# Kernel tuning notes

Hardware: AMD Instinct MI355X
Metric: run time of the kernel (lower is better)

## Reference

```python
import jax, jax.numpy as jnp
import numpy as np

N = 50000      # total nodes across batched graphs
E = 400000     # directed edges (before self-loops)
B = 256        # number of graphs / protein embeddings
F_IN = 78      # atom features (num_features_xd)
H1, F1 = 10, 78   # gcn1: heads=10, out=78 -> concat 780
F2 = 128       # gcn2 output_dim (heads=1)
EMB = 320      # PLM embed_dim
PLM = 128      # plm_layers[0]
BN_EPS = 1e-5


def setup_inputs() -> dict:
    key = jax.random.key(0)
    ks = jax.random.split(key, 30)
    g = lambda k, s, sc=0.05: (jax.random.normal(k, s, jnp.float32) * sc)
    inp = {
        'x': jax.random.normal(ks[0], (N, F_IN), jnp.float32),
        'edge_index': jax.random.randint(ks[1], (2, E), 0, N),
        # deterministic sorted assignment guarantees every graph id in [0,B) is populated
        'batch': (jnp.arange(N) * B) // N,
        'target_embedding': jax.random.normal(ks[2], (B, EMB), jnp.float32),
        # GATConv 1 (78 -> 78, heads=10, concat)
        'W1': g(ks[3], (F_IN, H1 * F1)), 'a1s': g(ks[4], (H1, F1)), 'a1d': g(ks[5], (H1, F1)), 'b1': g(ks[6], (H1 * F1,)),
        # GATConv 2 (780 -> 128, heads=1)
        'W2': g(ks[7], (H1 * F1, F2)), 'a2s': g(ks[8], (1, F2)), 'a2d': g(ks[9], (1, F2)), 'b2': g(ks[10], (F2,)),
        # fc_g1
        'Wg': g(ks[11], (F2, F2)), 'bg': g(ks[12], (F2,)),
        # PLM branch: Linear(320,128) + BatchNorm1d(128) in eval mode
        'Wxt': g(ks[13], (EMB, PLM)), 'bxt': g(ks[14], (PLM,)),
        'gamma': jnp.ones((PLM,), jnp.float32), 'beta': jnp.zeros((PLM,), jnp.float32),
        'rmean': g(ks[15], (PLM,)), 'rvar': jax.random.uniform(ks[16], (PLM,), jnp.float32, 0.5, 1.5),
        # head MLP
        'Wf1': g(ks[17], (F2 + PLM, 1024)), 'bf1': g(ks[18], (1024,)),
        'Wf2': g(ks[19], (1024, 256)), 'bf2': g(ks[20], (256,)),
        'Wo': g(ks[21], (256, 1)), 'bo': g(ks[22], (1,)),
    }
    return inp


def gat_conv(x, src, dst, W, a_s, a_d, b, n):
    """PyG-style GATConv (self-loops already included in src/dst)."""
    H, F = a_s.shape
    h = (x @ W).reshape(-1, H, F)                        # [n, H, F]
    e = jax.nn.leaky_relu((h * a_s).sum(-1)[src] + (h * a_d).sum(-1)[dst], 0.2)  # [e, H]
    m = jax.ops.segment_max(e, dst, num_segments=n)      # segment softmax over incoming edges
    p = jnp.exp(e - m[dst])
    denom = jax.ops.segment_sum(p, dst, num_segments=n)
    alpha = p / denom[dst]                               # [e, H]
    out = jax.ops.segment_sum(alpha[:, :, None] * h[src], dst, num_segments=n)  # [n, H, F]
    return out.reshape(-1, H * F) + b


def reference(x, edge_index, batch, target_embedding, W1, a1s, a1d, b1, W2, a2s, a2d, b2,
              Wg, bg, Wxt, bxt, gamma, beta, rmean, rvar, Wf1, bf1, Wf2, bf2, Wo, bo):
    n = x.shape[0]
    loop = jnp.arange(n)
    src = jnp.concatenate([edge_index[0], loop])   # add self-loops (GATConv default)
    dst = jnp.concatenate([edge_index[1], loop])
    h = jax.nn.elu(gat_conv(x, src, dst, W1, a1s, a1d, b1, n))      # [N, 780]
    h = jax.nn.relu(gat_conv(h, src, dst, W2, a2s, a2d, b2, n))     # [N, 128]
    g = jax.ops.segment_max(h, batch, num_segments=B)               # global max pool [B, 128]
    g = jax.nn.relu(g @ Wg + bg)
    xt = target_embedding @ Wxt + bxt
    xt = jax.nn.relu((xt - rmean) / jnp.sqrt(rvar + BN_EPS) * gamma + beta)  # BN eval
    xc = jnp.concatenate([g, xt], axis=1)                           # [B, 256]
    xc = jax.nn.relu(xc @ Wf1 + bf1)
    xc = jax.nn.relu(xc @ Wf2 + bf2)
    return xc @ Wo + bo                                             # [B, 1]
```

## Files before the change

kernel.cpp:

```cpp
#include <hip/hip_runtime.h>
#include <hip/hip_fp16.h>
#include <math.h>

static constexpr int F2 = 128, EMB = 320;

typedef _Float16 h8v __attribute__((ext_vector_type(8)));
typedef float f4v __attribute__((ext_vector_type(4)));

union F4H2 { float4 f; __half2 h[4]; };
union F2H2 { float2 f; __half2 h[2]; };

__device__ __forceinline__ __half2 shfl_xor_h2(__half2 v, int off) {
    union { __half2 h; float f; } u;
    u.h = v;
    u.f = __shfl_xor(u.f, off);
    return u.h;
}

__device__ __forceinline__ void esd(const int* src, const int* dst, int E, int e, int& s, int& d) {
    if (e < E) { s = src[e]; d = dst[e]; }
    else       { s = e - E; d = s; }
}

__global__ void k_count(const int* __restrict__ src, const int* __restrict__ dst, int E, int Etot,
                        int* __restrict__ cnt) {
    int e = blockIdx.x * 256 + threadIdx.x;
    if (e >= Etot) return;
    int s, d;
    esd(src, dst, E, e, s, d);
    atomicAdd(&cnt[d], 1);
}

__global__ void k_scan1(const int* __restrict__ in, int* __restrict__ out, int* __restrict__ bsum,
                        int n) {
    __shared__ int tmp[256];
    int t = threadIdx.x;
    int gid = blockIdx.x * 256 + t;
    int v = gid < n ? in[gid] : 0;
    tmp[t] = v;
    __syncthreads();
    for (int off = 1; off < 256; off <<= 1) {
        int u = (t >= off) ? tmp[t - off] : 0;
        __syncthreads();
        tmp[t] += u;
        __syncthreads();
    }
    if (gid < n) out[gid] = tmp[t] - v;
    if (t == 255) bsum[blockIdx.x] = tmp[255];
}

__global__ void k_scan2(int* __restrict__ bsum, int nb) {
    __shared__ int tmp[256];
    __shared__ int carry;
    int t = threadIdx.x;
    if (t == 0) carry = 0;
    __syncthreads();
    for (int base = 0; base < nb; base += 256) {
        int i = base + t;
        int v = (i < nb) ? bsum[i] : 0;
        tmp[t] = v;
        __syncthreads();
        for (int off = 1; off < 256; off <<= 1) {
            int u = (t >= off) ? tmp[t - off] : 0;
            __syncthreads();
            tmp[t] += u;
            __syncthreads();
        }
        if (i < nb) bsum[i] = tmp[t] - v + carry;
        __syncthreads();
        if (t == 0) carry += tmp[255];
        __syncthreads();
    }
}

__global__ void k_scan3(int* __restrict__ out, const int* __restrict__ bsum, int n, int Etot,
                        int* __restrict__ rp_last, int* __restrict__ cur) {
    int gid = blockIdx.x * 256 + threadIdx.x;
    if (gid < n) {
        int v = out[gid] + bsum[blockIdx.x];
        out[gid] = v;
        cur[gid] = v;
    }
    if (gid == 0) rp_last[0] = Etot;
}

__global__ void k_scatter(const int* __restrict__ src, const int* __restrict__ dst, int E, int Etot,
                          int* __restrict__ cur, int* __restrict__ csrc) {
    int e = blockIdx.x * 256 + threadIdx.x;
    if (e >= Etot) return;
    int s, d;
    esd(src, dst, E, e, s, d);
    int pos = atomicAdd(&cur[d], 1);
    csrc[pos] = s;
}

__global__ void k_prep_w(const float* __restrict__ W1, const float* __restrict__ a1s,
                         const float* __restrict__ a1d, const float* __restrict__ W2,
                         __half* __restrict__ W1T, float* __restrict__ wes,
                         float* __restrict__ wed, __half* __restrict__ W2T) {
    int idx = blockIdx.x * 256 + threadIdx.x;
    if (idx < 76800) {
        int h = idx / (80 * 96), r = idx % (80 * 96), c = r / 96, k = r % 96;
        float v = (c < 78 && k < 78) ? W1[(size_t)k * 780 + h * 78 + c] : 0.f;
        W1T[idx] = __float2half(v);
    } else if (idx < 77600) {
        int j = idx - 76800;
        int h = j / 80, k = j % 80;
        float s = 0.f, d = 0.f;
        if (k < 78) {
            for (int f = 0; f < 78; f++) {
                float w = W1[(size_t)k * 780 + h * 78 + f];
                s = fmaf(w, a1s[h * 78 + f], s);
                d = fmaf(w, a1d[h * 78 + f], d);
            }
        }
        wes[j] = s;
        wed[j] = d;
    } else if (idx < 77600 + 128 * 800) {
        int j = idx - 77600;
        int c = j / 800, k = j % 800;
        float v = (k < 780) ? W2[(size_t)k * 128 + c] : 0.f;
        W2T[j] = __float2half(v);
    }
}

__global__ void k_prep_xpk(const float* __restrict__ x, __half2* __restrict__ xpk, int N) {
    int idx = blockIdx.x * 256 + threadIdx.x;
    if (idx >= N * 64) return;
    int n = idx >> 6, l = idx & 63;
    float lo = x[(size_t)n * 78 + l];
    float hi = (64 + l < 78) ? x[(size_t)n * 78 + 64 + l] : 0.f;
    xpk[idx] = __floats2half2_rn(lo, hi);
}

__global__ void k_coefx(const float* __restrict__ x, const float* __restrict__ wes,
                        const float* __restrict__ wed, float* __restrict__ esg,
                        float* __restrict__ edg, int N) {
    int n = blockIdx.x * 256 + threadIdx.x;
    if (n >= N) return;
    float es[10] = {}, ed[10] = {};
    const float* xr = x + (size_t)n * 78;
    for (int k = 0; k < 78; k++) {
        float xv = xr[k];
#pragma unroll
        for (int h = 0; h < 10; h++) {
            es[h] = fmaf(xv, wes[h * 80 + k], es[h]);
            ed[h] = fmaf(xv, wed[h * 80 + k], ed[h]);
        }
    }
#pragma unroll
    for (int h = 0; h < 10; h++) {
        esg[(size_t)n * 16 + h] = es[h];
        edg[(size_t)n * 16 + h] = ed[h];
    }
}

__global__ void k_gatx10(const int* __restrict__ rp, const int* __restrict__ csrc,
                         const float* __restrict__ esg, const float* __restrict__ edg,
                         const __half2* __restrict__ xpk, __half* __restrict__ xagg, int N) {
    __shared__ __align__(16) __half2 pl[4][64][12];
    __shared__ __align__(16) int sl[4][64];
    int w = threadIdx.x >> 6, lane = threadIdx.x & 63;
    int node = blockIdx.x * 4 + w;
    if (node >= N) return;
    int beg = rp[node], end = rp[node + 1];
    int deg = end - beg;

    float edn[10];
    {
        const float* ep = edg + (size_t)node * 16;
        float4 a = *(const float4*)ep, b = *(const float4*)(ep + 4);
        float2 c = *(const float2*)(ep + 8);
        edn[0] = a.x; edn[1] = a.y; edn[2] = a.z; edn[3] = a.w;
        edn[4] = b.x; edn[5] = b.y; edn[6] = b.z; edn[7] = b.w;
        edn[8] = c.x; edn[9] = c.y;
    }

    __half2 acc[10];
#pragma unroll
    for (int h = 0; h < 10; h++) acc[h] = __floats2half2_rn(0.f, 0.f);

#define PASSC_BODY(LIMIT)                                                          \
    for (int i0 = 0; i0 < (LIMIT); i0 += 4) {                                      \
        int4 s4 = *(const int4*)&sl[w][i0];                                        \
        __half2 xr0 = xpk[(size_t)s4.x * 64 + lane];                               \
        __half2 xr1 = xpk[(size_t)s4.y * 64 + lane];                               \
        __half2 xr2 = xpk[(size_t)s4.z * 64 + lane];                               \
        __half2 xr3 = xpk[(size_t)s4.w * 64 + lane];                               \
        _Pragma("unroll")                                                          \
        for (int j = 0; j < 4; j++) {                                              \
            F4H2 qa, qb; F2H2 qc;                                                  \
            qa.f = *(const float4*)&pl[w][i0 + j][0];                              \
            qb.f = *(const float4*)&pl[w][i0 + j][4];                              \
            qc.f = *(const float2*)&pl[w][i0 + j][8];                              \
            __half2 xr = (j == 0) ? xr0 : (j == 1) ? xr1 : (j == 2) ? xr2 : xr3;   \
            acc[0] = __hfma2(qa.h[0], xr, acc[0]);                                 \
            acc[1] = __hfma2(qa.h[1], xr, acc[1]);                                 \
            acc[2] = __hfma2(qa.h[2], xr, acc[2]);                                 \
            acc[3] = __hfma2(qa.h[3], xr, acc[3]);                                 \
            acc[4] = __hfma2(qb.h[0], xr, acc[4]);                                 \
            acc[5] = __hfma2(qb.h[1], xr, acc[5]);                                 \
            acc[6] = __hfma2(qb.h[2], xr, acc[6]);                                 \
            acc[7] = __hfma2(qb.h[3], xr, acc[7]);                                 \
            acc[8] = __hfma2(qc.h[0], xr, acc[8]);                                 \
            acc[9] = __hfma2(qc.h[1], xr, acc[9]);                                 \
        }                                                                          \
    }

#define STASH(PVEC)                                                                \
    {                                                                              \
        F4H2 wa, wb; F2H2 wc;                                                      \
        _Pragma("unroll")                                                          \
        for (int h = 0; h < 4; h++) wa.h[h] = __float2half2_rn(PVEC[h]);           \
        _Pragma("unroll")                                                          \
        for (int h = 0; h < 4; h++) wb.h[h] = __float2half2_rn(PVEC[4 + h]);       \
        wc.h[0] = __float2half2_rn(PVEC[8]);                                       \
        wc.h[1] = __float2half2_rn(PVEC[9]);                                       \
        *(float4*)&pl[w][lane][0] = wa.f;                                          \
        *(float4*)&pl[w][lane][4] = wb.f;                                          \
        *(float2*)&pl[w][lane][8] = wc.f;                                          \
        sl[w][lane] = s;                                                           \
    }

    if (deg <= 64) {
        bool act = lane < deg;
        int s = act ? csrc[beg + lane] : 0;
        float p[10];
        if (act) {
            const float* sp = esg + (size_t)s * 16;
            float4 a = *(const float4*)sp, b = *(const float4*)(sp + 4);
            float2 c = *(const float2*)(sp + 8);
            float v[10];
            v[0] = a.x + edn[0]; v[1] = a.y + edn[1]; v[2] = a.z + edn[2]; v[3] = a.w + edn[3];
            v[4] = b.x + edn[4]; v[5] = b.y + edn[5]; v[6] = b.z + edn[6]; v[7] = b.w + edn[7];
            v[8] = c.x + edn[8]; v[9] = c.y + edn[9];
#pragma unroll
            for (int h = 0; h < 10; h++) {
                float vv = v[h] >= 0.f ? v[h] : 0.2f * v[h];
                p[h] = __expf(vv);
            }
        } else {
#pragma unroll
            for (int h = 0; h < 10; h++) p[h] = 0.f;
        }
        __half2 sh[5];
#pragma unroll
        for (int j = 0; j < 5; j++) sh[j] = __floats2half2_rn(p[2 * j], p[2 * j + 1]);
        int start = (deg <= 16) ? 8 : 32;
        for (int off = start; off; off >>= 1) {
#pragma unroll
            for (int j = 0; j < 5; j++) sh[j] = __hadd2(sh[j], shfl_xor_h2(sh[j], off));
        }
#pragma unroll
        for (int j = 0; j < 5; j++) {
            float2 f = __half22float2(sh[j]);
            p[2 * j] *= 1.f / f.x;
            p[2 * j + 1] *= 1.f / f.y;
        }
        STASH(p)
        PASSC_BODY(deg)
    } else {
        float ssf[10] = {};
        for (int cb = beg; cb < end; cb += 64) {
            int e = cb + lane;
            bool act = e < end;
            int si = act ? csrc[e] : 0;
            if (act) {
                const float* sp = esg + (size_t)si * 16;
#pragma unroll
                for (int h = 0; h < 10; h++) {
                    float vv = sp[h] + edn[h];
                    vv = vv >= 0.f ? vv : 0.2f * vv;
                    ssf[h] += __expf(vv);
                }
            }
        }
#pragma unroll
        for (int off = 32; off; off >>= 1) {
#pragma unroll
            for (int h = 0; h < 10; h++) ssf[h] += __shfl_xor(ssf[h], off);
        }
        float inv[10];
#pragma unroll
        for (int h = 0; h < 10; h++) inv[h] = 1.f / ssf[h];

        for (int cb = beg; cb < end; cb += 64) {
            int cnt = min(64, end - cb);
            int e = cb + lane;
            bool act = e < end;
            int s = act ? csrc[e] : 0;
            float p[10];
            if (act) {
                const float* sp = esg + (size_t)s * 16;
#pragma unroll
                for (int h = 0; h < 10; h++) {
                    float vv = sp[h] + edn[h];
                    vv = vv >= 0.f ? vv : 0.2f * vv;
                    p[h] = __expf(vv) * inv[h];
                }
            } else {
#pragma unroll
                for (int h = 0; h < 10; h++) p[h] = 0.f;
            }
            STASH(p)
            PASSC_BODY(cnt)
        }
    }
#undef PASSC_BODY
#undef STASH

    __half* op = xagg + (size_t)node * 800;
#pragma unroll
    for (int h = 0; h < 10; h++) {
        __half* hp = op + h * 80;
        hp[lane] = __low2half(acc[h]);
        if (lane < 16) hp[64 + lane] = __high2half(acc[h]);
    }
}

__global__ __launch_bounds__(512) void k_gemmQ(const __half* __restrict__ xagg,
                                               const __half* __restrict__ W1T,
                                               const float* __restrict__ b1,
                                               const __half* __restrict__ W2T,
                                               const float* __restrict__ a2s,
                                               const float* __restrict__ a2d,
                                               __half* __restrict__ h216,
                                               float* __restrict__ es2,
                                               float* __restrict__ ed2, int N) {
    constexpr int LQ = 808;
    __shared__ __align__(16) _Float16 qlds[32 * LQ];
    int w = threadIdx.x >> 6, lane = threadIdx.x & 63;
    int row0 = blockIdx.x * 32;
    int col16 = lane & 15, grp = lane >> 4;
    int ko = grp * 8;
    int rbase = grp * 4;

    for (int i = threadIdx.x; i < 32 * 28; i += 512) {
        int r = i / 28, c = 780 + i % 28;
        qlds[r * LQ + c] = (_Float16)0.f;
    }

    for (int j = w; j < 20; j += 8) {
        int h = j >> 1, half = j & 1;
        int ar = min(row0 + half * 16 + col16, N - 1);
        const _Float16* Ap = (const _Float16*)xagg + (size_t)ar * 800 + h * 80 + ko;
        const _Float16* Bp = (const _Float16*)W1T + ((size_t)h * 80 + col16) * 96 + ko;
        f4v acc1[5] = {};
#pragma unroll
        for (int ks = 0; ks < 3; ks++) {
            h8v a = *(const h8v*)(Ap + ks * 32);
#pragma unroll
            for (int t = 0; t < 5; t++) {
                h8v b = *(const h8v*)(Bp + (size_t)t * 16 * 96 + ks * 32);
                acc1[t] = __builtin_amdgcn_mfma_f32_16x16x32_f16(a, b, acc1[t], 0, 0, 0);
            }
        }
#pragma unroll
        for (int t = 0; t < 5; t++) {
            int c = t * 16 + col16;
            if (c < 78) {
                float bias = b1[h * 78 + c];
#pragma unroll
                for (int r = 0; r < 4; r++) {
                    float v = acc1[t][r] + bias;
                    float e = v > 0.f ? v : (__expf(v) - 1.f);
                    qlds[(half * 16 + rbase + r) * LQ + h * 78 + c] = (_Float16)e;
                }
            }
        }
    }
    __syncthreads();

    f4v acc0 = {}, acc1 = {};
    const _Float16* Bq = (const _Float16*)W2T + ((size_t)w * 16 + col16) * 800 + ko;
    const _Float16* Aq0 = qlds + (size_t)col16 * LQ + ko;
    const _Float16* Aq1 = qlds + (size_t)(16 + col16) * LQ + ko;
    for (int ks = 0; ks < 25; ks++) {
        h8v b = *(const h8v*)(Bq + ks * 32);
        h8v a0 = *(const h8v*)(Aq0 + ks * 32);
        h8v a1 = *(const h8v*)(Aq1 + ks * 32);
        acc0 = __builtin_amdgcn_mfma_f32_16x16x32_f16(a0, b, acc0, 0, 0, 0);
        acc1 = __builtin_amdgcn_mfma_f32_16x16x32_f16(a1, b, acc1, 0, 0, 0);
    }
    float wa = a2s[w * 16 + col16], wb = a2d[w * 16 + col16];
    float sse[2][4], ssd[2][4];
#pragma unroll
    for (int rb = 0; rb < 2; rb++) {
#pragma unroll
        for (int r = 0; r < 4; r++) {
            int n = row0 + rb * 16 + rbase + r;
            float v = rb ? acc1[r] : acc0[r];
            float se = v * wa, sd = v * wb;
#pragma unroll
            for (int off = 1; off < 16; off <<= 1) {
                se += __shfl_xor(se, off);
                sd += __shfl_xor(sd, off);
            }
            sse[rb][r] = se;
            ssd[rb][r] = sd;
            if (n < N) h216[(size_t)n * 128 + w * 16 + col16] = __float2half(v);
        }
    }
    __syncthreads();
    float* seredf = (float*)qlds;
    if (col16 == 0) {
#pragma unroll
        for (int rb = 0; rb < 2; rb++) {
#pragma unroll
            for (int r = 0; r < 4; r++) {
                int rowi = rb * 16 + rbase + r;
                seredf[w * 64 + rowi] = sse[rb][r];
                seredf[w * 64 + 32 + rowi] = ssd[rb][r];
            }
        }
    }
    __syncthreads();
    if (threadIdx.x < 32) {
        int n = row0 + threadIdx.x;
        if (n < N) {
            float es = 0.f, ed = 0.f;
#pragma unroll
            for (int ww = 0; ww < 8; ww++) {
                es += seredf[ww * 64 + threadIdx.x];
                ed += seredf[ww * 64 + 32 + threadIdx.x];
            }
            es2[n] = es;
            ed2[n] = ed;
        }
    }
}

__global__ void k_gatP(const int* __restrict__ rp, const int* __restrict__ csrc,
                       const float* __restrict__ es, const float* __restrict__ ed,
                       const __half2* __restrict__ h216, const float* __restrict__ b2,
                       const int* __restrict__ batch, unsigned* __restrict__ gb, int N) {
    __shared__ float red[4][128];
    __shared__ int bids[4];
    __shared__ __align__(16) __half2 plP[4][64];
    __shared__ __align__(16) int slP[4][64];
    int w = threadIdx.x >> 6, lane = threadIdx.x & 63;
    int node = blockIdx.x * 4 + w;
    bool valid = node < N;

    __half2 acc = __floats2half2_rn(0.f, 0.f);
    int bid = -1;

#define PASSC2(LIMIT)                                                      \
    for (int i0 = 0; i0 < (LIMIT); i0 += 4) {                              \
        int4 s4 = *(const int4*)&slP[w][i0];                               \
        F4H2 q; q.f = *(const float4*)&plP[w][i0];                         \
        __half2 f0 = h216[(size_t)s4.x * 64 + lane];                       \
        __half2 f1 = h216[(size_t)s4.y * 64 + lane];                       \
        __half2 f2 = h216[(size_t)s4.z * 64 + lane];                       \
        __half2 f3 = h216[(size_t)s4.w * 64 + lane];                       \
        acc = __hfma2(q.h[0], f0, acc);                                    \
        acc = __hfma2(q.h[1], f1, acc);                                    \
        acc = __hfma2(q.h[2], f2, acc);                                    \
        acc = __hfma2(q.h[3], f3, acc);                                    \
    }

    if (valid) {
        int beg = rp[node], end = rp[node + 1];
        int deg = end - beg;
        float edn = ed[node];
        bid = batch[node];

        if (deg <= 64) {
            bool act = lane < deg;
            int s = act ? csrc[beg + lane] : 0;
            float p = 0.f;
            if (act) {
                float v = es[s] + edn;
                v = v >= 0.f ? v : 0.2f * v;
                p = __expf(v);
            }
            float ss = p;
            int start = (deg <= 16) ? 8 : 32;
            for (int off = start; off; off >>= 1) ss += __shfl_xor(ss, off);
            p *= 1.f / ss;
            plP[w][lane] = __float2half2_rn(p);
            slP[w][lane] = s;
            PASSC2(deg)
        } else {
            float ss = 0.f;
            for (int cb = beg; cb < end; cb += 64) {
                int e = cb + lane;
                bool act = e < end;
                int s = act ? csrc[e] : 0;
                if (act) {
                    float v = es[s] + edn;
                    v = v >= 0.f ? v : 0.2f * v;
                    ss += __expf(v);
                }
            }
#pragma unroll
            for (int off = 32; off; off >>= 1) ss += __shfl_xor(ss, off);
            float inv = 1.f / ss;
            for (int cb = beg; cb < end; cb += 64) {
                int cnt = min(64, end - cb);
                int e = cb + lane;
                bool act = e < end;
                int s = act ? csrc[e] : 0;
                float p = 0.f;
                if (act) {
                    float v = es[s] + edn;
                    v = v >= 0.f ? v : 0.2f * v;
                    p = __expf(v) * inv;
                }
                plP[w][lane] = __float2half2_rn(p);
                slP[w][lane] = s;
                PASSC2(cnt)
            }
        }
    }
#undef PASSC2

    float2 af = __half22float2(acc);
    red[w][2 * lane]     = valid ? fmaxf(af.x + b2[2 * lane], 0.f) : 0.f;
    red[w][2 * lane + 1] = valid ? fmaxf(af.y + b2[2 * lane + 1], 0.f) : 0.f;
    if (lane == 0) bids[w] = valid ? bid : -1;
    __syncthreads();
    if (threadIdx.x < 128) {
        int c = threadIdx.x;
        int b0 = bids[0];
        bool same = (bids[1] == b0) && (bids[2] == b0) && (bids[3] == b0);
        if (same && b0 >= 0) {
            float m = fmaxf(fmaxf(red[0][c], red[1][c]), fmaxf(red[2][c], red[3][c]));
            atomicMax(&gb[(size_t)b0 * 128 + c], __float_as_uint(m));
        } else {
#pragma unroll
            for (int w2 = 0; w2 < 4; w2++) {
                if (bids[w2] >= 0)
                    atomicMax(&gb[(size_t)bids[w2] * 128 + c], __float_as_uint(red[w2][c]));
            }
        }
    }
}

__global__ void k_head_gxt(const unsigned* __restrict__ gbits, const float* __restrict__ Wg,
                           const float* __restrict__ bg, const float* __restrict__ te,
                           const float* __restrict__ Wxt, const float* __restrict__ bxt,
                           const float* __restrict__ gamma, const float* __restrict__ beta,
                           const float* __restrict__ rmean, const float* __restrict__ rvar,
                           float* __restrict__ xc) {
    __shared__ float sg[F2];
    __shared__ float st[EMB];
    int b = blockIdx.x, t = threadIdx.x;
    if (t < 128) {
        sg[t] = __uint_as_float(gbits[(size_t)b * F2 + t]);
    } else {
        for (int k = t - 128; k < EMB; k += 128) st[k] = te[(size_t)b * EMB + k];
    }
    __syncthreads();
    if (t < 128) {
        float acc = bg[t];
        for (int k = 0; k < F2; k++) acc = fmaf(sg[k], Wg[k * F2 + t], acc);
        xc[(size_t)b * 256 + t] = fmaxf(acc, 0.f);
    } else {
        int c = t - 128;
        float acc = bxt[c];
        for (int k = 0; k < EMB; k++) acc = fmaf(st[k], Wxt[k * F2 + c], acc);
        acc = (acc - rmean[c]) * rsqrtf(rvar[c] + 1e-5f) * gamma[c] + beta[c];
        xc[(size_t)b * 256 + 128 + c] = fmaxf(acc, 0.f);
    }
}

__global__ void k_head_mlp(const float* __restrict__ xc, const float* __restrict__ Wf1,
                           const float* __restrict__ bf1, const float* __restrict__ Wf2,
                           const float* __restrict__ bf2, const float* __restrict__ Wo,
                           const float* __restrict__ bo, float* __restrict__ out) {
    __shared__ float s0[256];
    __shared__ float s1[1024];
    int b = blockIdx.x, t = threadIdx.x;
    s0[t] = xc[(size_t)b * 256 + t];
    __syncthreads();
    for (int col = t; col < 1024; col += 256) {
        float acc = bf1[col];
        for (int k = 0; k < 256; k++) acc = fmaf(s0[k], Wf1[k * 1024 + col], acc);
        s1[col] = fmaxf(acc, 0.f);
    }
    __syncthreads();
    {
        float acc = bf2[t];
        for (int k = 0; k < 1024; k++) acc = fmaf(s1[k], Wf2[k * 256 + t], acc);
        float v = fmaxf(acc, 0.f);
        __syncthreads();
        s0[t] = v * Wo[t];
    }
    __syncthreads();
    if (t < 64) {
        float acc = s0[t] + s0[64 + t] + s0[128 + t] + s0[192 + t];
        for (int off = 32; off; off >>= 1) acc += __shfl_down(acc, off);
        if (t == 0) out[b] = acc + bo[0];
    }
}

extern "C" void kernel_launch(void* const* d_in, const int* in_sizes, int n_in,
                              void* d_out, int out_size, void* d_ws, size_t ws_size,
                              hipStream_t stream) {
    const float* x     = (const float*)d_in[0];
    const int*   ei    = (const int*)d_in[1];
    const int*   batch = (const int*)d_in[2];
    const float* te    = (const float*)d_in[3];
    const float* W1    = (const float*)d_in[4];
    const float* a1s   = (const float*)d_in[5];
    const float* a1d   = (const float*)d_in[6];
    const float* b1    = (const float*)d_in[7];
    const float* W2    = (const float*)d_in[8];
    const float* a2s   = (const float*)d_in[9];
    const float* a2d   = (const float*)d_in[10];
    const float* b2    = (const float*)d_in[11];
    const float* Wg    = (const float*)d_in[12];
    const float* bg    = (const float*)d_in[13];
    const float* Wxt   = (const float*)d_in[14];
    const float* bxt   = (const float*)d_in[15];
    const float* gamma = (const float*)d_in[16];
    const float* beta  = (const float*)d_in[17];
    const float* rmean = (const float*)d_in[18];
    const float* rvar  = (const float*)d_in[19];
    const float* Wf1   = (const float*)d_in[20];
    const float* bf1   = (const float*)d_in[21];
    const float* Wf2   = (const float*)d_in[22];
    const float* bf2   = (const float*)d_in[23];
    const float* Wo    = (const float*)d_in[24];
    const float* bo    = (const float*)d_in[25];

    const int N = in_sizes[0] / 78;
    const int E = in_sizes[1] / 2;
    const int B = in_sizes[3] / EMB;
    const int Etot = E + N;
    const int* src = ei;
    const int* dst = ei + E;

    char* p = (char*)d_ws;
    auto alloc = [&](size_t bytes) -> void* {
        void* r = p;
        p += (bytes + 255) & ~(size_t)255;
        return r;
    };
    __half2*  xpk  = (__half2*)alloc((size_t)N * 64 * 4);
    __half*   xagg = (__half*)alloc((size_t)N * 800 * 2 + 256);
    __half*   h216 = (__half*)alloc((size_t)N * 128 * 2);
    float*    esg  = (float*)alloc((size_t)N * 16 * 4);
    float*    edg  = (float*)alloc((size_t)N * 16 * 4);
    float*    es2  = (float*)alloc((size_t)N * 4);
    float*    ed2  = (float*)alloc((size_t)N * 4);
    __half*   W1T  = (__half*)alloc((size_t)10 * 80 * 96 * 2);
    __half*   W2T  = (__half*)alloc((size_t)128 * 800 * 2);
    float*    wes  = (float*)alloc((size_t)800 * 4);
    float*    wed  = (float*)alloc((size_t)800 * 4);
    int*      cnt  = (int*)alloc((size_t)N * 4);
    int*      rp   = (int*)alloc((size_t)(N + 1) * 4);
    int*      cur  = (int*)alloc((size_t)N * 4);
    int*      csrc = (int*)alloc((size_t)Etot * 4);
    int*      bsum = (int*)alloc((size_t)1024 * 4);
    unsigned* gb   = (unsigned*)alloc((size_t)B * F2 * 4);
    float*    xc   = (float*)alloc((size_t)B * 256 * 4);

    auto gsz = [](long long t) { return (int)((t + 255) / 256); };
    const int nb = gsz(N);
    const int nwave = (N + 3) / 4;
    const int nrow32 = (N + 31) / 32;

    hipMemsetAsync(cnt, 0, (size_t)N * 4, stream);
    k_count<<<gsz(Etot), 256, 0, stream>>>(src, dst, E, Etot, cnt);
    k_scan1<<<nb, 256, 0, stream>>>(cnt, rp, bsum, N);
    k_scan2<<<1, 256, 0, stream>>>(bsum, nb);
    k_scan3<<<nb, 256, 0, stream>>>(rp, bsum, N, Etot, rp + N, cur);
    k_scatter<<<gsz(Etot), 256, 0, stream>>>(src, dst, E, Etot, cur, csrc);

    k_prep_w<<<gsz(77600 + 128 * 800), 256, 0, stream>>>(W1, a1s, a1d, W2, W1T, wes, wed, W2T);
    k_prep_xpk<<<gsz((long long)N * 64), 256, 0, stream>>>(x, xpk, N);
    k_coefx<<<nb, 256, 0, stream>>>(x, wes, wed, esg, edg, N);
    hipMemsetAsync(gb, 0, (size_t)B * F2 * 4, stream);

    k_gatx10<<<nwave, 256, 0, stream>>>(rp, csrc, esg, edg, xpk, xagg, N);

    k_gemmQ<<<nrow32, 512, 0, stream>>>(xagg, W1T, b1, W2T, a2s, a2d, h216, es2, ed2, N);

    k_gatP<<<nwave, 256, 0, stream>>>(rp, csrc, es2, ed2, (const __half2*)h216, b2, batch, gb, N);

    k_head_gxt<<<B, 256, 0, stream>>>(gb, Wg, bg, te, Wxt, bxt, gamma, beta, rmean, rvar, xc);
    k_head_mlp<<<B, 256, 0, stream>>>(xc, Wf1, bf1, Wf2, bf2, Wo, bo, (float*)d_out);
}
```

Before: 311.3 us.

## Split head MLP into two column-parallel kernels with atomic output reduction

The single per-graph head MLP kernel (256 blocks doing both the 256x1024 and 1024x256 layers serially) is replaced by two kernels gridded over (graph, column tile). This gives four times more blocks, and each inner loop uses four independent accumulators to break the FMA dependency chain. The final dot with Wo is reduced per 64-column tile and summed into a zeroed output via atomicAdd. The cost is an extra launch, an f1o round trip through global memory, an output memset, and summation order that varies with atomic ordering.

New measurement: 294.7 us, median of 2. 5.3% less time.

```diff
diff --git a/kernel.cpp b/kernel.cpp
--- a/kernel.cpp
+++ b/kernel.cpp
@@ -565,33 +565,44 @@
     }
 }
 
-__global__ void k_head_mlp(const float* __restrict__ xc, const float* __restrict__ Wf1,
-                           const float* __restrict__ bf1, const float* __restrict__ Wf2,
+__global__ void k_head_f1(const float* __restrict__ xc, const float* __restrict__ Wf1,
+                          const float* __restrict__ bf1, float* __restrict__ f1o) {
+    __shared__ float srow[256];
+    int b = blockIdx.x, t = threadIdx.x;
+    srow[t] = xc[(size_t)b * 256 + t];
+    __syncthreads();
+    int col = blockIdx.y * 256 + t;
+    float a0 = 0.f, a1 = 0.f, a2 = 0.f, a3 = 0.f;
+    for (int k = 0; k < 256; k += 4) {
+        a0 = fmaf(srow[k + 0], Wf1[(size_t)(k + 0) * 1024 + col], a0);
+        a1 = fmaf(srow[k + 1], Wf1[(size_t)(k + 1) * 1024 + col], a1);
+        a2 = fmaf(srow[k + 2], Wf1[(size_t)(k + 2) * 1024 + col], a2);
+        a3 = fmaf(srow[k + 3], Wf1[(size_t)(k + 3) * 1024 + col], a3);
+    }
+    float acc = ((a0 + a1) + (a2 + a3)) + bf1[col];
+    f1o[(size_t)b * 1024 + col] = fmaxf(acc, 0.f);
+}
+
+__global__ void k_head_f2o(const float* __restrict__ f1o, const float* __restrict__ Wf2,
                            const float* __restrict__ bf2, const float* __restrict__ Wo,
                            const float* __restrict__ bo, float* __restrict__ out) {
-    __shared__ float s0[256];
-    __shared__ float s1[1024];
+    __shared__ float srow[1024];
     int b = blockIdx.x, t = threadIdx.x;
-    s0[t] = xc[(size_t)b * 256 + t];
-    __syncthreads();
-    for (int col = t; col < 1024; col += 256) {
-        float acc = bf1[col];
-        for (int k = 0; k < 256; k++) acc = fmaf(s0[k], Wf1[k * 1024 + col], acc);
-        s1[col] = fmaxf(acc, 0.f);
-    }
-    __syncthreads();
-    {
-        float acc = bf2[t];
-        for (int k = 0; k < 1024; k++) acc = fmaf(s1[k], Wf2[k * 256 + t], acc);
-        float v = fmaxf(acc, 0.f);
-        __syncthreads();
-        s0[t] = v * Wo[t];
-    }
-    __syncthreads();
-    if (t < 64) {
-        float acc = s0[t] + s0[64 + t] + s0[128 + t] + s0[192 + t];
-        for (int off = 32; off; off >>= 1) acc += __shfl_down(acc, off);
-        if (t == 0) out[b] = acc + bo[0];
+    for (int k = t; k < 1024; k += 64) srow[k] = f1o[(size_t)b * 1024 + k];
+    __syncthreads();
+    int col = blockIdx.y * 64 + t;
+    float a0 = 0.f, a1 = 0.f, a2 = 0.f, a3 = 0.f;
+    for (int k = 0; k < 1024; k += 4) {
+        a0 = fmaf(srow[k + 0], Wf2[(size_t)(k + 0) * 256 + col], a0);
+        a1 = fmaf(srow[k + 1], Wf2[(size_t)(k + 1) * 256 + col], a1);
+        a2 = fmaf(srow[k + 2], Wf2[(size_t)(k + 2) * 256 + col], a2);
+        a3 = fmaf(srow[k + 3], Wf2[(size_t)(k + 3) * 256 + col], a3);
+    }
+    float v = fmaxf(((a0 + a1) + (a2 + a3)) + bf2[col], 0.f) * Wo[col];
+    for (int off = 32; off; off >>= 1) v += __shfl_down(v, off);
+    if (t == 0) {
+        float add = v + (blockIdx.y == 0 ? bo[0] : 0.f);
+        atomicAdd(&out[b], add);
     }
 }
 
@@ -656,6 +667,7 @@
     int*      bsum = (int*)alloc((size_t)1024 * 4);
     unsigned* gb   = (unsigned*)alloc((size_t)B * F2 * 4);
     float*    xc   = (float*)alloc((size_t)B * 256 * 4);
+    float*    f1o  = (float*)alloc((size_t)B * 1024 * 4);
 
     auto gsz = [](long long t) { return (int)((t + 255) / 256); };
     const int nb = gsz(N);
@@ -673,6 +685,7 @@
     k_prep_xpk<<<gsz((long long)N * 64), 256, 0, stream>>>(x, xpk, N);
     k_coefx<<<nb, 256, 0, stream>>>(x, wes, wed, esg, edg, N);
     hipMemsetAsync(gb, 0, (size_t)B * F2 * 4, stream);
+    hipMemsetAsync(d_out, 0, (size_t)out_size * 4, stream);
 
     k_gatx10<<<nwave, 256, 0, stream>>>(rp, csrc, esg, edg, xpk, xagg, N);
 
@@ -681,5 +694,6 @@
     k_gatP<<<nwave, 256, 0, stream>>>(rp, csrc, es2, ed2, (const __half2*)h216, b2, batch, gb, N);
 
     k_head_gxt<<<B, 256, 0, stream>>>(gb, Wg, bg, te, Wxt, bxt, gamma, beta, rmean, rvar, xc);
-    k_head_mlp<<<B, 256, 0, stream>>>(xc, Wf1, bf1, Wf2, bf2, Wo, bo, (float*)d_out);
-}
+    k_head_f1<<<dim3(B, 4), 256, 0, stream>>>(xc, Wf1, bf1, f1o);
+    k_head_f2o<<<dim3(B, 4), 64, 0, stream>>>(f1o, Wf2, bf2, Wo, bo, (float*)d_out);
+}
```
